# Performance work log

Hardware: AMD Instinct MI355X
Metric: run time of the kernel (lower is better)

Reference implementation:

```python
import jax, jax.numpy as jnp
import numpy as np

B, N, CIN, H, UNITS = 8, 2048, 256, 256, 256


def setup_inputs() -> dict:
    key = jax.random.key(0)
    ks = jax.random.split(key, 7)
    s = 1.0 / np.sqrt(CIN)
    return {
        "x": jax.random.normal(ks[0], (B, N, CIN), dtype=jnp.float32),
        "Wq": jax.random.normal(ks[1], (CIN, H), dtype=jnp.float32) * s,
        "bq": jax.random.normal(ks[2], (H,), dtype=jnp.float32) * 0.01,
        "Wk": jax.random.normal(ks[3], (CIN, H), dtype=jnp.float32) * s,
        "bk": jax.random.normal(ks[4], (H,), dtype=jnp.float32) * 0.01,
        "Wm": jax.random.normal(ks[5], (H, UNITS), dtype=jnp.float32) * (1.0 / np.sqrt(H)),
        "bm": jax.random.normal(ks[6], (UNITS,), dtype=jnp.float32) * 0.01,
    }


def reference(x, Wq, bq, Wk, bk, Wm, bm):
    # Dense projections with fused relu (as in the Keras module)
    q = jax.nn.relu(x @ Wq + bq)          # (B,N,H)
    k = jax.nn.relu(x @ Wk + bk)          # (B,N,H)
    v = q                                 # NOTE: source uses fc_query for value (fc_value unused)
    # Unscaled key @ query^T, softmax over last axis
    kq = jax.nn.softmax(jnp.einsum('bnh,bmh->bnm', k, q), axis=-1)  # (B,N,N)
    # value^T @ kq, then Permute((2,1)): att[b,m,h] = sum_n v[b,n,h] * kq[b,n,m]
    att = jnp.einsum('bnh,bnm->bmh', v, kq)                          # (B,N,H)
    return jax.nn.relu(att @ Wm + bm)                                # (B,N,UNITS)
```

## Files before the change

### kernel.cpp

```cpp
#include <hip/hip_runtime.h>
#include <hip/hip_bf16.h>
#include <math.h>

#define BB   8
#define NN   2048
#define CC   256
#define MTOT (BB * NN)

typedef __bf16 bf16_t;
typedef bf16_t    bf16x8 __attribute__((ext_vector_type(8)));
typedef _Float16  halfx8 __attribute__((ext_vector_type(8)));
typedef float     floatx4 __attribute__((ext_vector_type(4)));

#define LOG2E 1.44269504088896f

__device__ __forceinline__ void gl_lds16(const bf16_t* g, bf16_t* l) {
    __builtin_amdgcn_global_load_lds(
        (const __attribute__((address_space(1))) unsigned int*)g,
        (__attribute__((address_space(3))) unsigned int*)l, 16, 0, 0);
}

template<int OMODE, bool BIASRELU, bool DO_STATS>
__global__ __launch_bounds__(256, 3)
void gemm_nt(const bf16_t* __restrict__ A, const bf16_t* __restrict__ B,
             void* __restrict__ C, const float* __restrict__ bias,
             int lda, int ldb, int ldc,
             long strideA, long strideB, long strideC,
             float* __restrict__ pm, float* __restrict__ pl)
{
    const int b = blockIdx.z;
    A += (long)b * strideA;
    B += (long)b * strideB;
    const int m0 = blockIdx.y * 128;
    const int n0 = blockIdx.x * 128;

    __shared__ bf16_t As[128 * 64];
    __shared__ bf16_t Bs[128 * 64];
    __shared__ float  smx[4][4][16];
    __shared__ float  ssm[4][4][16];

    const int tid  = threadIdx.x;
    const int wid  = tid >> 6, lane = tid & 63;
    const int wm   = (wid >> 1) * 64, wn = (wid & 1) * 64;
    const int fr   = lane & 15;
    const int u16  = lane >> 4;
    const int fsw  = fr & 7;

    floatx4 acc[4][4] = {};

    for (int k0 = 0; k0 < 256; k0 += 64) {
#pragma unroll
        for (int r = 0; r < 4; ++r) {
            const int lin = tid + r * 256;
            const int rw  = lin >> 3, kc = lin & 7;
            const int kcs = kc ^ (rw & 7);
            gl_lds16(A + (long)(m0 + rw) * lda + k0 + kcs * 8, As + lin * 8);
            gl_lds16(B + (long)(n0 + rw) * ldb + k0 + kcs * 8, Bs + lin * 8);
        }
        __syncthreads();
        bf16x8 af[4][2], bf[4][2];
#pragma unroll
        for (int f = 0; f < 4; ++f)
#pragma unroll
            for (int j = 0; j < 2; ++j) {
                const int chunk = (j * 4 + u16) ^ fsw;
                af[f][j] = *(const bf16x8*)(As + (wm + f * 16 + fr) * 64 + chunk * 8);
                bf[f][j] = *(const bf16x8*)(Bs + (wn + f * 16 + fr) * 64 + chunk * 8);
            }
#pragma unroll
        for (int j = 0; j < 2; ++j)
#pragma unroll
            for (int f = 0; f < 4; ++f)
#pragma unroll
                for (int g = 0; g < 4; ++g)
                    acc[f][g] = __builtin_amdgcn_mfma_f32_16x16x32_bf16(af[f][j], bf[g][j], acc[f][g], 0, 0, 0);
        __syncthreads();
    }

    const int rbase = u16 * 4;
#pragma unroll
    for (int g = 0; g < 4; ++g) {
        const int n = n0 + wn + g * 16 + fr;
        const float bv = BIASRELU ? bias[n] : 0.0f;
#pragma unroll
        for (int f = 0; f < 4; ++f) {
#pragma unroll
            for (int r = 0; r < 4; ++r) {
                const int m = m0 + wm + f * 16 + rbase + r;
                float v = acc[f][g][r] + bv;
                if (BIASRELU) v = v > 0.0f ? v : 0.0f;
                if (OMODE == 0)
                    ((float*)C)[(long)b * strideC + (long)m * ldc + n] = v;
                else if (OMODE == 1)
                    ((bf16_t*)C)[(long)b * strideC + (long)m * ldc + n] = (bf16_t)v;
                else
                    ((_Float16*)C)[(long)b * strideC + (long)m * ldc + n] = (_Float16)v;
            }
        }
    }

    if (DO_STATS) {
        float lmax[4], lsum[4];
#pragma unroll
        for (int g = 0; g < 4; ++g) {
            float m = -1e30f;
#pragma unroll
            for (int f = 0; f < 4; ++f)
#pragma unroll
                for (int r = 0; r < 4; ++r) m = fmaxf(m, acc[f][g][r]);
            m = fmaxf(m, __shfl_xor(m, 16));
            m = fmaxf(m, __shfl_xor(m, 32));
            float s = 0.0f;
#pragma unroll
            for (int f = 0; f < 4; ++f)
#pragma unroll
                for (int r = 0; r < 4; ++r) s += __expf(acc[f][g][r] - m);
            s += __shfl_xor(s, 16);
            s += __shfl_xor(s, 32);
            lmax[g] = m; lsum[g] = s;
        }
        if (lane < 16) {
#pragma unroll
            for (int g = 0; g < 4; ++g) {
                smx[wid][g][lane] = lmax[g];
                ssm[wid][g][lane] = lsum[g];
            }
        }
        __syncthreads();
        if (tid < 128) {
            const int pair = tid >> 6;
            const int idx  = tid & 63;
            const int g = idx >> 4, f2 = idx & 15;
            const float m0v = smx[pair][g][f2], m1v = smx[pair + 2][g][f2];
            const float M = fmaxf(m0v, m1v);
            const float L = ssm[pair][g][f2] * __expf(m0v - M) +
                            ssm[pair + 2][g][f2] * __expf(m1v - M);
            const int n = n0 + pair * 64 + g * 16 + f2;
            const long o = ((long)b * 16 + blockIdx.y) * NN + n;
            pm[o] = M;
            pl[o] = L;
        }
    }
}

__global__ __launch_bounds__(256)
void stats_combine(const float* __restrict__ pm, const float* __restrict__ pl,
                   float* __restrict__ c2)
{
    const int i = blockIdx.x * 256 + threadIdx.x;
    const int b = i >> 11, n = i & 2047;
    float M = -1e30f, L = 0.0f;
#pragma unroll
    for (int t = 0; t < 16; ++t) {
        const long o = ((long)b * 16 + t) * NN + n;
        const float m = pm[o], l = pl[o];
        const float nm = fmaxf(M, m);
        L = L * __expf(M - nm) + l * __expf(m - nm);
        M = nm;
    }
    c2[i] = (M + logf(L)) * LOG2E;
}

#define APAD 68
__global__ __launch_bounds__(256, 2)
void att_out(const _Float16* __restrict__ St, const bf16_t* __restrict__ qmT,
             const float* __restrict__ c2, const float* __restrict__ bm,
             float* __restrict__ out)
{
    const int b  = blockIdx.z;
    const int m0 = blockIdx.x * 32;
    const _Float16* S  = St  + (long)b * NN * NN;
    const bf16_t*   Q  = qmT + (long)b * 256 * NN;
    const float*    C2 = c2  + b * NN;
    float*          O  = out + (long)b * NN * 256;

    __shared__ bf16_t As[32 * APAD];
    __shared__ bf16_t Bs[256 * 64];

    const int tid  = threadIdx.x;
    const int wid  = tid >> 6, lane = tid & 63;
    const int wm2  = (wid >> 1) * 16;
    const int wu   = (wid & 1) * 128;
    const int fr   = lane & 15;
    const int u16  = lane >> 4;
    const int kb   = u16 * 8;
    const int fsw  = fr & 7;
    const int arow = tid >> 3;
    const int aseg = tid & 7;

    const _Float16* Srow = S + (long)(m0 + arow) * NN + aseg * 8;

    floatx4 acc[8] = {};

    for (int n0 = 0; n0 < NN; n0 += 64) {
#pragma unroll
        for (int r = 0; r < 8; ++r) {
            const int lin = tid + r * 256;
            const int rw  = lin >> 3, kc = lin & 7;
            const int kcs = kc ^ (rw & 7);
            gl_lds16(Q + (long)rw * NN + n0 + kcs * 8, Bs + lin * 8);
        }
        const halfx8 hv = *(const halfx8*)(Srow + n0);
        const float4 ca = *(const float4*)(C2 + n0 + aseg * 8);
        const float4 cb = *(const float4*)(C2 + n0 + aseg * 8 + 4);
        bf16x8 p;
        p[0] = (bf16_t)exp2f(fmaf((float)hv[0], LOG2E, -ca.x));
        p[1] = (bf16_t)exp2f(fmaf((float)hv[1], LOG2E, -ca.y));
        p[2] = (bf16_t)exp2f(fmaf((float)hv[2], LOG2E, -ca.z));
        p[3] = (bf16_t)exp2f(fmaf((float)hv[3], LOG2E, -ca.w));
        p[4] = (bf16_t)exp2f(fmaf((float)hv[4], LOG2E, -cb.x));
        p[5] = (bf16_t)exp2f(fmaf((float)hv[5], LOG2E, -cb.y));
        p[6] = (bf16_t)exp2f(fmaf((float)hv[6], LOG2E, -cb.z));
        p[7] = (bf16_t)exp2f(fmaf((float)hv[7], LOG2E, -cb.w));
        *(bf16x8*)(As + arow * APAD + aseg * 8) = p;
        __syncthreads();

        bf16x8 af[2], bg[8][2];
#pragma unroll
        for (int j = 0; j < 2; ++j)
            af[j] = *(const bf16x8*)(As + (wm2 + fr) * APAD + j * 32 + kb);
#pragma unroll
        for (int g = 0; g < 8; ++g)
#pragma unroll
            for (int j = 0; j < 2; ++j) {
                const int chunk = (j * 4 + u16) ^ fsw;
                bg[g][j] = *(const bf16x8*)(Bs + (wu + g * 16 + fr) * 64 + chunk * 8);
            }
#pragma unroll
        for (int j = 0; j < 2; ++j)
#pragma unroll
            for (int g = 0; g < 8; ++g)
                acc[g] = __builtin_amdgcn_mfma_f32_16x16x32_bf16(af[j], bg[g][j], acc[g], 0, 0, 0);
        __syncthreads();
    }

    const int rbase = u16 * 4;
#pragma unroll
    for (int g = 0; g < 8; ++g) {
        const int u = wu + g * 16 + fr;
        const float bvv = bm[u];
#pragma unroll
        for (int r = 0; r < 4; ++r) {
            const int m = m0 + wm2 + rbase + r;
            const float v = acc[g][r] + bvv;
            O[(long)m * 256 + u] = v > 0.0f ? v : 0.0f;
        }
    }
}

__global__ __launch_bounds__(256)
void cvt_bf16(const float* __restrict__ x, bf16_t* __restrict__ y)
{
    const long i = ((long)blockIdx.x * 256 + threadIdx.x) * 8;
    const float4 a = *(const float4*)(x + i);
    const float4 b = *(const float4*)(x + i + 4);
    bf16x8 o;
    o[0] = (bf16_t)a.x; o[1] = (bf16_t)a.y; o[2] = (bf16_t)a.z; o[3] = (bf16_t)a.w;
    o[4] = (bf16_t)b.x; o[5] = (bf16_t)b.y; o[6] = (bf16_t)b.z; o[7] = (bf16_t)b.w;
    *(bf16x8*)(y + i) = o;
}

__global__ __launch_bounds__(256)
void prep_w(const float* __restrict__ Wq, const float* __restrict__ Wk,
            const float* __restrict__ Wm, const float* __restrict__ bq,
            const float* __restrict__ bk, bf16_t* __restrict__ WqkT,
            bf16_t* __restrict__ WmT, float* __restrict__ bqk)
{
    const int z = blockIdx.z;
    const float* W = (z == 0) ? Wq : (z == 1) ? Wk : Wm;
    bf16_t* Wt = (z == 0) ? WqkT : (z == 1) ? (WqkT + 256 * 256) : WmT;
    __shared__ float t[32][33];
    const int n0 = blockIdx.x * 32, k0 = blockIdx.y * 32;
    const int tx = threadIdx.x & 31, ty = threadIdx.x >> 5;
    for (int i = ty; i < 32; i += 8) t[i][tx] = W[(k0 + i) * 256 + n0 + tx];
    __syncthreads();
    for (int i = ty; i < 32; i += 8) Wt[(n0 + i) * 256 + k0 + tx] = (bf16_t)t[tx][i];
    if (z == 0 && blockIdx.x == 0 && blockIdx.y == 0) {
        bqk[threadIdx.x]       = bq[threadIdx.x];
        bqk[256 + threadIdx.x] = bk[threadIdx.x];
    }
}

extern "C" void kernel_launch(void* const* d_in, const int* in_sizes, int n_in,
                              void* d_out, int out_size, void* d_ws, size_t ws_size,
                              hipStream_t stream)
{
    (void)in_sizes; (void)n_in; (void)out_size; (void)ws_size;
    const float* x  = (const float*)d_in[0];
    const float* Wq = (const float*)d_in[1];
    const float* bq = (const float*)d_in[2];
    const float* Wk = (const float*)d_in[3];
    const float* bk = (const float*)d_in[4];
    const float* Wm = (const float*)d_in[5];
    const float* bm = (const float*)d_in[6];
    float* out = (float*)d_out;

    char* w = (char*)d_ws;
    _Float16* St   = (_Float16*)w;                  w += (size_t)BB * NN * NN * 2;
    bf16_t* x_bf   = (bf16_t*)w;                    w += (size_t)MTOT * 256 * 2;
    bf16_t* qk     = (bf16_t*)w;                    w += (size_t)MTOT * 512 * 2;
    bf16_t* qmT    = (bf16_t*)w;                    w += (size_t)MTOT * 256 * 2;
    bf16_t* WqkT   = (bf16_t*)w;                    w += 512 * 256 * 2;
    bf16_t* WmT    = (bf16_t*)w;                    w += 256 * 256 * 2;
    float*  bqk    = (float*)w;                     w += 512 * 4;
    float*  pm     = (float*)w;                     w += (size_t)BB * 16 * NN * 4;
    float*  pl     = (float*)w;                     w += (size_t)BB * 16 * NN * 4;
    float*  c2b    = (float*)w;

    cvt_bf16<<<dim3(MTOT * 256 / (256 * 8)), 256, 0, stream>>>(x, x_bf);
    prep_w<<<dim3(8, 8, 3), 256, 0, stream>>>(Wq, Wk, Wm, bq, bk, WqkT, WmT, bqk);

    gemm_nt<1, true, false><<<dim3(4, 128, 1), 256, 0, stream>>>(
        x_bf, WqkT, qk, bqk, 256, 256, 512, 0, 0, 0, nullptr, nullptr);

    gemm_nt<1, false, false><<<dim3(16, 2, BB), 256, 0, stream>>>(
        WmT, qk, qmT, nullptr, 256, 512, NN,
        0, (long)NN * 512, (long)256 * NN, nullptr, nullptr);

    gemm_nt<2, false, true><<<dim3(16, 16, BB), 256, 0, stream>>>(
        qk, qk + 256, St, nullptr, 512, 512, NN,
        (long)NN * 512, (long)NN * 512, (long)NN * NN, pm, pl);

    stats_combine<<<dim3(MTOT / 256), 256, 0, stream>>>(pm, pl, c2b);

    att_out<<<dim3(64, 1, BB), 256, 0, stream>>>(St, qmT, c2b, bm, out);
}
```

Measured before the change: 180.1 us.

## Split att_out over output columns and interleave batch index in block ids

att_out now splits the 256 output units into two 128-wide halves per block. This doubles the grid to 1024 blocks, halves the LDS tile and accumulators, and raises the occupancy hint to 4. Blocks for the batched GEMMs and att_out are launched on a flat grid with the batch index taken from the low bits, which spreads batches across XCDs/CUs. The cost is that each S row tile is read and exponentiated twice, once per output half, which adds global traffic and exp work.

```diff
diff --git a/kernel.cpp b/kernel.cpp
--- a/kernel.cpp
+++ b/kernel.cpp
@@ -24,15 +24,25 @@
 __global__ __launch_bounds__(256, 3)
 void gemm_nt(const bf16_t* __restrict__ A, const bf16_t* __restrict__ B,
              void* __restrict__ C, const float* __restrict__ bias,
-             int lda, int ldb, int ldc,
+             int lda, int ldb, int ldc, int swz,
              long strideA, long strideB, long strideC,
              float* __restrict__ pm, float* __restrict__ pl)
 {
-    const int b = blockIdx.z;
+    int b, m0, n0, myi;
+    if (swz) {
+        b = blockIdx.x & 7;
+        const int r = blockIdx.x >> 3;
+        n0  = (r % swz) * 128;
+        myi = r / swz;
+        m0  = myi * 128;
+    } else {
+        b   = blockIdx.z;
+        m0  = blockIdx.y * 128;
+        n0  = blockIdx.x * 128;
+        myi = blockIdx.y;
+    }
     A += (long)b * strideA;
     B += (long)b * strideB;
-    const int m0 = blockIdx.y * 128;
-    const int n0 = blockIdx.x * 128;
 
     __shared__ bf16_t As[128 * 64];
     __shared__ bf16_t Bs[128 * 64];
@@ -136,7 +146,7 @@
             const float L = ssm[pair][g][f2] * __expf(m0v - M) +
                             ssm[pair + 2][g][f2] * __expf(m1v - M);
             const int n = n0 + pair * 64 + g * 16 + f2;
-            const long o = ((long)b * 16 + blockIdx.y) * NN + n;
+            const long o = ((long)b * 16 + myi) * NN + n;
             pm[o] = M;
             pl[o] = L;
         }
@@ -162,25 +172,28 @@
 }
 
 #define APAD 68
-__global__ __launch_bounds__(256, 2)
+__global__ __launch_bounds__(256, 4)
 void att_out(const _Float16* __restrict__ St, const bf16_t* __restrict__ qmT,
              const float* __restrict__ c2, const float* __restrict__ bm,
              float* __restrict__ out)
 {
-    const int b  = blockIdx.z;
-    const int m0 = blockIdx.x * 32;
+    const int bid = blockIdx.x;
+    const int b   = bid & 7;
+    const int r   = bid >> 3;
+    const int m0  = (r >> 1) * 32;
+    const int u0  = (r & 1) * 128;
     const _Float16* S  = St  + (long)b * NN * NN;
     const bf16_t*   Q  = qmT + (long)b * 256 * NN;
     const float*    C2 = c2  + b * NN;
     float*          O  = out + (long)b * NN * 256;
 
     __shared__ bf16_t As[32 * APAD];
-    __shared__ bf16_t Bs[256 * 64];
+    __shared__ bf16_t Bs[128 * 64];
 
     const int tid  = threadIdx.x;
     const int wid  = tid >> 6, lane = tid & 63;
     const int wm2  = (wid >> 1) * 16;
-    const int wu   = (wid & 1) * 128;
+    const int wu   = (wid & 1) * 64;
     const int fr   = lane & 15;
     const int u16  = lane >> 4;
     const int kb   = u16 * 8;
@@ -190,15 +203,15 @@
 
     const _Float16* Srow = S + (long)(m0 + arow) * NN + aseg * 8;
 
-    floatx4 acc[8] = {};
+    floatx4 acc[4] = {};
 
     for (int n0 = 0; n0 < NN; n0 += 64) {
 #pragma unroll
-        for (int r = 0; r < 8; ++r) {
-            const int lin = tid + r * 256;
+        for (int r2 = 0; r2 < 4; ++r2) {
+            const int lin = tid + r2 * 256;
             const int rw  = lin >> 3, kc = lin & 7;
             const int kcs = kc ^ (rw & 7);
-            gl_lds16(Q + (long)rw * NN + n0 + kcs * 8, Bs + lin * 8);
+            gl_lds16(Q + (long)(u0 + rw) * NN + n0 + kcs * 8, Bs + lin * 8);
         }
         const halfx8 hv = *(const halfx8*)(Srow + n0);
         const float4 ca = *(const float4*)(C2 + n0 + aseg * 8);
@@ -215,12 +228,12 @@
         *(bf16x8*)(As + arow * APAD + aseg * 8) = p;
         __syncthreads();
 
-        bf16x8 af[2], bg[8][2];
+        bf16x8 af[2], bg[4][2];
 #pragma unroll
         for (int j = 0; j < 2; ++j)
             af[j] = *(const bf16x8*)(As + (wm2 + fr) * APAD + j * 32 + kb);
 #pragma unroll
-        for (int g = 0; g < 8; ++g)
+        for (int g = 0; g < 4; ++g)
 #pragma unroll
             for (int j = 0; j < 2; ++j) {
                 const int chunk = (j * 4 + u16) ^ fsw;
@@ -229,20 +242,20 @@
 #pragma unroll
         for (int j = 0; j < 2; ++j)
 #pragma unroll
-            for (int g = 0; g < 8; ++g)
+            for (int g = 0; g < 4; ++g)
                 acc[g] = __builtin_amdgcn_mfma_f32_16x16x32_bf16(af[j], bg[g][j], acc[g], 0, 0, 0);
         __syncthreads();
     }
 
     const int rbase = u16 * 4;
 #pragma unroll
-    for (int g = 0; g < 8; ++g) {
-        const int u = wu + g * 16 + fr;
+    for (int g = 0; g < 4; ++g) {
+        const int u = u0 + wu + g * 16 + fr;
         const float bvv = bm[u];
 #pragma unroll
-        for (int r = 0; r < 4; ++r) {
-            const int m = m0 + wm2 + rbase + r;
-            const float v = acc[g][r] + bvv;
+        for (int r2 = 0; r2 < 4; ++r2) {
+            const int m = m0 + wm2 + rbase + r2;
+            const float v = acc[g][r2] + bvv;
             O[(long)m * 256 + u] = v > 0.0f ? v : 0.0f;
         }
     }
@@ -311,17 +324,17 @@
     prep_w<<<dim3(8, 8, 3), 256, 0, stream>>>(Wq, Wk, Wm, bq, bk, WqkT, WmT, bqk);
 
     gemm_nt<1, true, false><<<dim3(4, 128, 1), 256, 0, stream>>>(
-        x_bf, WqkT, qk, bqk, 256, 256, 512, 0, 0, 0, nullptr, nullptr);
-
-    gemm_nt<1, false, false><<<dim3(16, 2, BB), 256, 0, stream>>>(
-        WmT, qk, qmT, nullptr, 256, 512, NN,
+        x_bf, WqkT, qk, bqk, 256, 256, 512, 0, 0, 0, 0, nullptr, nullptr);
+
+    gemm_nt<1, false, false><<<dim3(256, 1, 1), 256, 0, stream>>>(
+        WmT, qk, qmT, nullptr, 256, 512, NN, 16,
         0, (long)NN * 512, (long)256 * NN, nullptr, nullptr);
 
-    gemm_nt<2, false, true><<<dim3(16, 16, BB), 256, 0, stream>>>(
-        qk, qk + 256, St, nullptr, 512, 512, NN,
+    gemm_nt<2, false, true><<<dim3(2048, 1, 1), 256, 0, stream>>>(
+        qk, qk + 256, St, nullptr, 512, 512, NN, 16,
         (long)NN * 512, (long)NN * 512, (long)NN * NN, pm, pl);
 
     stats_combine<<<dim3(MTOT / 256), 256, 0, stream>>>(pm, pl, c2b);
 
-    att_out<<<dim3(64, 1, BB), 256, 0, stream>>>(St, qmT, c2b, bm, out);
-}
+    att_out<<<dim3(1024, 1, 1), 256, 0, stream>>>(St, qmT, c2b, bm, out);
+}
```

After: 172.9 us. 4.0% less time.
